# Kernel tuning notes

Measured on AMD Instinct MI355X. Metric: run time of the kernel, lower is better.

## Reference

```python
import jax, jax.numpy as jnp
import numpy as np

SIZE_SUBMAP = 1024          # points per submap (module global in repo)
RATIO = 0.5                 # CONFIG['Detector']['ratio']
K_POS = int(SIZE_SUBMAP * RATIO)  # 512
K = 32                      # self.k, fps ratio = K / K_POS
B = 2048                    # number of submaps in batch


def fps_single(pts, k):
    """Deterministic farthest point sampling (start at index 0). pts: [n,3] -> [k] int indices."""
    min_d = jnp.sum((pts - pts[0]) ** 2, axis=-1)  # [n]

    def step(min_d, _):
        idx = jnp.argmax(min_d)
        d2 = jnp.sum((pts - pts[idx]) ** 2, axis=-1)
        return jnp.minimum(min_d, d2), idx

    _, idxs = jax.lax.scan(step, min_d, None, length=k - 1)
    return jnp.concatenate([jnp.zeros((1,), dtype=idxs.dtype), idxs])


def setup_inputs() -> dict:
    key = jax.random.key(0)
    ks = jax.random.split(key, 8)
    n = B * SIZE_SUBMAP
    x = jax.random.normal(ks[0], (n, 32), jnp.float32)
    pos = jax.random.normal(ks[1], (n, 3), jnp.float32) * 10.0
    batch = jnp.repeat(jnp.arange(B, dtype=jnp.int32), SIZE_SUBMAP)
    # MLP([32,16,8]) -> Linear(8,1) -> Softplus
    W1 = jax.random.normal(ks[2], (32, 16), jnp.float32) / np.sqrt(32.0)
    b1 = jnp.zeros((16,), jnp.float32)
    W2 = jax.random.normal(ks[3], (16, 8), jnp.float32) / np.sqrt(16.0)
    b2 = jnp.zeros((8,), jnp.float32)
    W3 = jax.random.normal(ks[4], (8, 1), jnp.float32) / np.sqrt(8.0)
    b3 = jnp.zeros((1,), jnp.float32)
    return {"x": x, "pos": pos, "batch": batch,
            "W1": W1, "b1": b1, "W2": W2, "b2": b2, "W3": W3, "b3": b3}


def reference(x, pos, batch, W1, b1, W2, b2, W3, b3):
    bsz = batch.shape[0] // SIZE_SUBMAP  # static batch_size (= batch.max()+1)
    # small per-point MLP + Softplus score
    h = jax.nn.relu(x @ W1 + b1)
    h = jax.nn.relu(h @ W2 + b2)
    s = jax.nn.softplus(h @ W3 + b3)          # [B*N, 1]
    x_batch = s.reshape(bsz, -1)               # [B, N]
    pos_b = pos.reshape(bsz, -1, 3)            # [B, N, 3]
    # distance of xy-coords to submap center
    dist = jnp.linalg.norm(pos_b[..., :2], axis=-1)     # [B, N]
    # k_pos closest points (topk of -dist)
    _, idx1 = jax.lax.top_k(-dist, K_POS)               # [B, K_POS]
    pos_sel = jnp.take_along_axis(pos_b, idx1[..., None], axis=1)  # [B, K_POS, 3]
    # batched farthest point sampling, K points per submap (within-batch indices)
    key_idx = jax.vmap(lambda p: fps_single(p, K))(pos_sel)        # [B, K]
    original_indices = jnp.take_along_axis(idx1, key_idx, axis=1)  # [B, K]
    weights = jnp.take_along_axis(x_batch, original_indices, axis=1)  # [B, K]
    return weights, original_indices
```

## Files before the change

### kernel.cpp

```cpp
#include <hip/hip_runtime.h>
#include <math.h>
#include <stdint.h>

#define N_PTS 1024
#define K_POS 512
#define K_FPS 32

typedef unsigned long long u64;
typedef unsigned int u32;

__device__ __forceinline__ u64 shfl_xor_u64(u64 v, int mask) {
    return __shfl_xor(v, mask, 64);
}

__global__ __launch_bounds__(512) void sort_kernel(
    const float* __restrict__ pos,
    float4* __restrict__ ws)
{
#pragma clang fp contract(off)
    const int b   = blockIdx.x;
    const int tid = threadIdx.x;
    __shared__ u64 key[N_PTS];

    const float* pb = pos + (size_t)b * N_PTS * 3;

    u64 v0, v1;
    {
        float x = pb[tid * 3 + 0];
        float y = pb[tid * 3 + 1];
        float xx = x * x, yy = y * y;
        float d = sqrtf(xx + yy);
        v0 = ((u64)__float_as_uint(d) << 32) | (u32)tid;
        int i = tid + 512;
        x = pb[i * 3 + 0];
        y = pb[i * 3 + 1];
        xx = x * x; yy = y * y;
        d = sqrtf(xx + yy);
        v1 = ((u64)__float_as_uint(d) << 32) | (u32)i;
    }

    const int i0 = tid, i1 = tid + 512;
    for (int k = 2; k <= N_PTS; k <<= 1) {
        const bool up0 = ((i0 & k) == 0);
        const bool up1 = ((i1 & k) == 0);
        for (int j = k >> 1; j > 0; j >>= 1) {
            if (j == 512) {
                u64 lo = (v0 < v1) ? v0 : v1;
                u64 hi = (v0 < v1) ? v1 : v0;
                v0 = lo; v1 = hi;
            } else if (j >= 64) {
                key[i0] = v0; key[i1] = v1;
                __syncthreads();
                u64 o0 = key[i0 ^ j];
                u64 o1 = key[i1 ^ j];
                bool keep0 = (((i0 & j) == 0) == up0);
                bool keep1 = (((i1 & j) == 0) == up1);
                v0 = ((v0 < o0) == keep0) ? v0 : o0;
                v1 = ((v1 < o1) == keep1) ? v1 : o1;
                __syncthreads();
            } else {
                u64 o0 = shfl_xor_u64(v0, j);
                u64 o1 = shfl_xor_u64(v1, j);
                bool keep0 = (((i0 & j) == 0) == up0);
                bool keep1 = (((i1 & j) == 0) == up1);
                v0 = ((v0 < o0) == keep0) ? v0 : o0;
                v1 = ((v1 < o1) == keep1) ? v1 : o1;
            }
        }
    }

    int orig = (int)(u32)(v0 & 0xffffffffu);
    float x = pb[orig * 3 + 0];
    float y = pb[orig * 3 + 1];
    float z = pb[orig * 3 + 2];
    ws[(size_t)b * K_POS + tid] = make_float4(x, y, z, (float)orig);
}

__global__ __launch_bounds__(256) void fps_wave_kernel(
    const float4* __restrict__ ws,
    float* __restrict__ out_idx,
    int B)
{
#pragma clang fp contract(off)
    const int lane = threadIdx.x & 63;
    const int b    = blockIdx.x * 4 + (threadIdx.x >> 6);
    if (b >= B) return;

    const float4* wsb = ws + (size_t)b * K_POS;
    float px[8], py[8], pz[8], pidx[8], mind[8];
    #pragma unroll
    for (int r = 0; r < 8; ++r) {
        float4 p = wsb[r * 64 + lane];
        px[r] = p.x; py[r] = p.y; pz[r] = p.z; pidx[r] = p.w;
    }

    float wx = __shfl(px[0], 0, 64);
    float wy = __shfl(py[0], 0, 64);
    float wz = __shfl(pz[0], 0, 64);
    float wi = __shfl(pidx[0], 0, 64);

    float* ob = out_idx + (size_t)b * K_FPS;
    if (lane == 0) ob[0] = wi;

    #pragma unroll
    for (int r = 0; r < 8; ++r) {
        float dx = px[r] - wx, dy = py[r] - wy, dz = pz[r] - wz;
        float u0 = dx * dx, u1 = dy * dy, u2 = dz * dz;
        mind[r] = (u0 + u1) + u2;
    }

    for (int it = 1; it < K_FPS; ++it) {
        u64 best = 0;
        #pragma unroll
        for (int r = 0; r < 8; ++r) {
            int e = r * 64 + lane;
            u64 kk = ((u64)__float_as_uint(mind[r]) << 32) |
                     (u64)(0xffffffffu - (u32)e);
            if (kk > best) best = kk;
        }
        #pragma unroll
        for (int off = 32; off > 0; off >>= 1) {
            u64 o = shfl_xor_u64(best, off);
            if (o > best) best = o;
        }
        int ew = (int)(0xffffffffu - (u32)(best & 0xffffffffu));
        int rw = ew >> 6, lw = ew & 63;
        float sx = 0.f, sy = 0.f, sz = 0.f, si = 0.f;
        #pragma unroll
        for (int r = 0; r < 8; ++r)
            if (r == rw) { sx = px[r]; sy = py[r]; sz = pz[r]; si = pidx[r]; }
        wx = __shfl(sx, lw, 64);
        wy = __shfl(sy, lw, 64);
        wz = __shfl(sz, lw, 64);
        wi = __shfl(si, lw, 64);
        if (lane == 0) ob[it] = wi;

        #pragma unroll
        for (int r = 0; r < 8; ++r) {
            float dx = px[r] - wx, dy = py[r] - wy, dz = pz[r] - wz;
            float u0 = dx * dx, u1 = dy * dy, u2 = dz * dz;
            float d2 = (u0 + u1) + u2;
            mind[r] = fminf(mind[r], d2);
        }
    }
}

__global__ __launch_bounds__(256) void mlp_kernel(
    const float* __restrict__ x,
    const float* __restrict__ W1, const float* __restrict__ b1,
    const float* __restrict__ W2, const float* __restrict__ b2,
    const float* __restrict__ W3, const float* __restrict__ b3,
    const float* __restrict__ idx_f,
    float* __restrict__ out_w, int total)
{
    __shared__ float sW1[32 * 16];
    __shared__ float sW2[16 * 8];
    __shared__ float sW3[8];
    __shared__ float sb1[16];
    __shared__ float sb2[8];
    __shared__ float sb3;

    for (int i = threadIdx.x; i < 512; i += 256) sW1[i] = W1[i];
    if (threadIdx.x < 128) sW2[threadIdx.x] = W2[threadIdx.x];
    if (threadIdx.x < 16)  sb1[threadIdx.x] = b1[threadIdx.x];
    if (threadIdx.x < 8) {
        sb2[threadIdx.x] = b2[threadIdx.x];
        sW3[threadIdx.x] = W3[threadIdx.x];
    }
    if (threadIdx.x == 0) sb3 = b3[0];
    __syncthreads();

    int t = blockIdx.x * 256 + threadIdx.x;
    if (t >= total) return;

    int b    = t >> 5;
    int orig = (int)(idx_f[t] + 0.5f);
    const float* xr = x + ((size_t)b * N_PTS + (size_t)orig) * 32;

    float xi[32];
    #pragma unroll
    for (int i = 0; i < 32; i += 4) {
        float4 v = *(const float4*)(xr + i);
        xi[i] = v.x; xi[i + 1] = v.y; xi[i + 2] = v.z; xi[i + 3] = v.w;
    }

    float h1[16];
    #pragma unroll
    for (int j = 0; j < 16; ++j) {
        float a = sb1[j];
        #pragma unroll
        for (int i = 0; i < 32; ++i) a += xi[i] * sW1[i * 16 + j];
        h1[j] = fmaxf(a, 0.0f);
    }
    float h2[8];
    #pragma unroll
    for (int j = 0; j < 8; ++j) {
        float a = sb2[j];
        #pragma unroll
        for (int i = 0; i < 16; ++i) a += h1[i] * sW2[i * 8 + j];
        h2[j] = fmaxf(a, 0.0f);
    }
    float v = sb3;
    #pragma unroll
    for (int i = 0; i < 8; ++i) v += h2[i] * sW3[i];

    float sp = fmaxf(v, 0.0f) + log1pf(expf(-fabsf(v)));
    out_w[t] = sp;
}

extern "C" void kernel_launch(void* const* d_in, const int* in_sizes, int n_in,
                              void* d_out, int out_size, void* d_ws, size_t ws_size,
                              hipStream_t stream) {
    const float* x   = (const float*)d_in[0];
    const float* pos = (const float*)d_in[1];
    const float* W1 = (const float*)d_in[3];
    const float* b1 = (const float*)d_in[4];
    const float* W2 = (const float*)d_in[5];
    const float* b2 = (const float*)d_in[6];
    const float* W3 = (const float*)d_in[7];
    const float* b3 = (const float*)d_in[8];

    const int B = in_sizes[2] / N_PTS;
    float* out_w = (float*)d_out;
    float* out_i = (float*)d_out + (size_t)B * K_FPS;
    float4* ws   = (float4*)d_ws;

    sort_kernel<<<B, 512, 0, stream>>>(pos, ws);
    fps_wave_kernel<<<(B + 3) / 4, 256, 0, stream>>>(ws, out_i, B);

    const int total = B * K_FPS;
    mlp_kernel<<<(total + 255) / 256, 256, 0, stream>>>(
        x, W1, b1, W2, b2, W3, b3, out_i, out_w, total);
}
```

Measured before the change: 395.2 us.

## Fuse bitonic sort into FPS kernel with per-wave register sort

Merges the sort and FPS kernels into one kernel where each wavefront sorts one submap's 1024 keys entirely in registers (16 keys per lane), using lane shuffles for cross-lane stages and in-register compare-exchange for cross-register stages. This drops the shared-memory bitonic stages, the barriers and the workspace round-trip between kernels, as well as one launch. The trade is higher register pressure (16 u64 keys per lane) and more shuffle instructions per wave, which may lower occupancy. It also adds scattered global gathers of the selected points.

After: 392.8 us. About the same (-0.6%).

```diff
diff --git a/kernel.cpp b/kernel.cpp
--- a/kernel.cpp
+++ b/kernel.cpp
@@ -13,71 +13,36 @@
     return __shfl_xor(v, mask, 64);
 }
 
-__global__ __launch_bounds__(512) void sort_kernel(
+__device__ __forceinline__ void shuffle_stage(u64 key[16], int j, int k, int lane) {
+    #pragma unroll
+    for (int r = 0; r < 16; ++r) {
+        int e = (r << 6) | lane;
+        u64 o = shfl_xor_u64(key[r], j);
+        bool up      = ((e & k) == 0);
+        bool lowhalf = ((lane & j) == 0);
+        bool keep = ((key[r] < o) == (lowhalf == up));
+        key[r] = keep ? key[r] : o;
+    }
+}
+
+template<int JR, int KR>
+__device__ __forceinline__ void intra_stage(u64 key[16]) {
+    #pragma unroll
+    for (int r = 0; r < 16; ++r) {
+        if ((r & JR) == 0) {
+            const int r2 = r | JR;
+            const bool up = ((r & KR) == 0);
+            u64 a = key[r], c = key[r2];
+            u64 lo = (a < c) ? a : c;
+            u64 hi = (a < c) ? c : a;
+            key[r]  = up ? lo : hi;
+            key[r2] = up ? hi : lo;
+        }
+    }
+}
+
+__global__ __launch_bounds__(256) void sortfps_kernel(
     const float* __restrict__ pos,
-    float4* __restrict__ ws)
-{
-#pragma clang fp contract(off)
-    const int b   = blockIdx.x;
-    const int tid = threadIdx.x;
-    __shared__ u64 key[N_PTS];
-
-    const float* pb = pos + (size_t)b * N_PTS * 3;
-
-    u64 v0, v1;
-    {
-        float x = pb[tid * 3 + 0];
-        float y = pb[tid * 3 + 1];
-        float xx = x * x, yy = y * y;
-        float d = sqrtf(xx + yy);
-        v0 = ((u64)__float_as_uint(d) << 32) | (u32)tid;
-        int i = tid + 512;
-        x = pb[i * 3 + 0];
-        y = pb[i * 3 + 1];
-        xx = x * x; yy = y * y;
-        d = sqrtf(xx + yy);
-        v1 = ((u64)__float_as_uint(d) << 32) | (u32)i;
-    }
-
-    const int i0 = tid, i1 = tid + 512;
-    for (int k = 2; k <= N_PTS; k <<= 1) {
-        const bool up0 = ((i0 & k) == 0);
-        const bool up1 = ((i1 & k) == 0);
-        for (int j = k >> 1; j > 0; j >>= 1) {
-            if (j == 512) {
-                u64 lo = (v0 < v1) ? v0 : v1;
-                u64 hi = (v0 < v1) ? v1 : v0;
-                v0 = lo; v1 = hi;
-            } else if (j >= 64) {
-                key[i0] = v0; key[i1] = v1;
-                __syncthreads();
-                u64 o0 = key[i0 ^ j];
-                u64 o1 = key[i1 ^ j];
-                bool keep0 = (((i0 & j) == 0) == up0);
-                bool keep1 = (((i1 & j) == 0) == up1);
-                v0 = ((v0 < o0) == keep0) ? v0 : o0;
-                v1 = ((v1 < o1) == keep1) ? v1 : o1;
-                __syncthreads();
-            } else {
-                u64 o0 = shfl_xor_u64(v0, j);
-                u64 o1 = shfl_xor_u64(v1, j);
-                bool keep0 = (((i0 & j) == 0) == up0);
-                bool keep1 = (((i1 & j) == 0) == up1);
-                v0 = ((v0 < o0) == keep0) ? v0 : o0;
-                v1 = ((v1 < o1) == keep1) ? v1 : o1;
-            }
-        }
-    }
-
-    int orig = (int)(u32)(v0 & 0xffffffffu);
-    float x = pb[orig * 3 + 0];
-    float y = pb[orig * 3 + 1];
-    float z = pb[orig * 3 + 2];
-    ws[(size_t)b * K_POS + tid] = make_float4(x, y, z, (float)orig);
-}
-
-__global__ __launch_bounds__(256) void fps_wave_kernel(
-    const float4* __restrict__ ws,
     float* __restrict__ out_idx,
     int B)
 {
@@ -86,12 +51,46 @@
     const int b    = blockIdx.x * 4 + (threadIdx.x >> 6);
     if (b >= B) return;
 
-    const float4* wsb = ws + (size_t)b * K_POS;
+    const float* pb = pos + (size_t)b * N_PTS * 3;
+
+    u64 key[16];
+    #pragma unroll
+    for (int r = 0; r < 16; ++r) {
+        int e = (r << 6) | lane;
+        float x = pb[e * 3 + 0];
+        float y = pb[e * 3 + 1];
+        float xx = x * x, yy = y * y;
+        float d = sqrtf(xx + yy);
+        key[r] = ((u64)__float_as_uint(d) << 32) | (u32)e;
+    }
+
+    for (int k = 2; k <= 64; k <<= 1)
+        for (int j = k >> 1; j > 0; j >>= 1)
+            shuffle_stage(key, j, k, lane);
+    intra_stage<1, 2>(key);
+    for (int j = 32; j > 0; j >>= 1) shuffle_stage(key, j, 128, lane);
+    intra_stage<2, 4>(key);
+    intra_stage<1, 4>(key);
+    for (int j = 32; j > 0; j >>= 1) shuffle_stage(key, j, 256, lane);
+    intra_stage<4, 8>(key);
+    intra_stage<2, 8>(key);
+    intra_stage<1, 8>(key);
+    for (int j = 32; j > 0; j >>= 1) shuffle_stage(key, j, 512, lane);
+    intra_stage<8, 16>(key);
+    intra_stage<4, 16>(key);
+    intra_stage<2, 16>(key);
+    intra_stage<1, 16>(key);
+    for (int j = 32; j > 0; j >>= 1) shuffle_stage(key, j, 1024, lane);
+
+
     float px[8], py[8], pz[8], pidx[8], mind[8];
     #pragma unroll
     for (int r = 0; r < 8; ++r) {
-        float4 p = wsb[r * 64 + lane];
-        px[r] = p.x; py[r] = p.y; pz[r] = p.z; pidx[r] = p.w;
+        int orig = (int)(u32)(key[r] & 0xffffffffu);
+        px[r] = pb[orig * 3 + 0];
+        py[r] = pb[orig * 3 + 1];
+        pz[r] = pb[orig * 3 + 2];
+        pidx[r] = (float)orig;
     }
 
     float wx = __shfl(px[0], 0, 64);
@@ -223,10 +222,8 @@
     const int B = in_sizes[2] / N_PTS;
     float* out_w = (float*)d_out;
     float* out_i = (float*)d_out + (size_t)B * K_FPS;
-    float4* ws   = (float4*)d_ws;
-
-    sort_kernel<<<B, 512, 0, stream>>>(pos, ws);
-    fps_wave_kernel<<<(B + 3) / 4, 256, 0, stream>>>(ws, out_i, B);
+
+    sortfps_kernel<<<(B + 3) / 4, 256, 0, stream>>>(pos, out_i, B);
 
     const int total = B * K_FPS;
     mlp_kernel<<<(total + 255) / 256, 256, 0, stream>>>(
```
